# Kernel tuning notes

Hardware: AMD Instinct MI355X
Metric: run time of the kernel (lower is better)

The kernel has to match this reference:

```python
import jax, jax.numpy as jnp
import numpy as np

N_NODES = 100000   # m for both sparse matmuls (graph adjacency is N x N)
ITERATIONS = 10
ALPHA = 0.1
N_FEATURES = 2000
HIDDEN = 64
N_LABELS = 16
NNZ_FEAT = 5000000
N_EDGES = 3200000


def setup_inputs() -> dict:
    key = jax.random.key(0)
    ks = jax.random.split(key, 10)
    feat_rows = jax.random.randint(ks[0], (NNZ_FEAT,), 0, N_NODES, dtype=jnp.int32)
    feat_cols = jax.random.randint(ks[1], (NNZ_FEAT,), 0, N_FEATURES, dtype=jnp.int32)
    feature_values = jax.random.uniform(ks[2], (NNZ_FEAT,), dtype=jnp.float32)
    edge_rows = jax.random.randint(ks[3], (N_EDGES,), 0, N_NODES, dtype=jnp.int32)
    edge_cols = jax.random.randint(ks[4], (N_EDGES,), 0, N_NODES, dtype=jnp.int32)
    edge_weights = jax.random.uniform(ks[5], (N_EDGES,), dtype=jnp.float32) * (1.0 / 32.0)
    W1 = jax.random.normal(ks[6], (N_FEATURES, HIDDEN), dtype=jnp.float32) * 0.05
    b1 = jax.random.normal(ks[7], (HIDDEN,), dtype=jnp.float32) * 0.05
    W2 = jax.random.normal(ks[8], (HIDDEN, N_LABELS), dtype=jnp.float32) * 0.1
    b2 = jax.random.normal(ks[9], (N_LABELS,), dtype=jnp.float32) * 0.1
    return {"feat_rows": feat_rows, "feat_cols": feat_cols, "feature_values": feature_values,
            "edge_rows": edge_rows, "edge_cols": edge_cols, "edge_weights": edge_weights,
            "W1": W1, "b1": b1, "W2": W2, "b2": b2}


def spmm(rows, cols, vals, matrix, m):
    # sparse [m, k] (COO) @ dense [k, d]: gather rows of dense, scale, scatter-add
    out = matrix[cols] * vals[:, None]          # [nnz, d]
    return jax.ops.segment_sum(out, rows, num_segments=m)


def reference(feat_rows, feat_cols, feature_values, edge_rows, edge_cols,
              edge_weights, W1, b1, W2, b2):
    # layer 1: sparse features [N, F] @ W1 [F, H] + b1  (eval mode: dropout is identity)
    latent1 = spmm(feat_rows, feat_cols, feature_values, W1, N_NODES) + b1  # [N, H]
    latent1 = jax.nn.relu(latent1)
    z = latent1 @ W2 + b2                       # [N, L] local predictions

    def step(p, _):
        new = spmm(edge_rows, edge_cols, edge_weights, p, N_NODES)  # A_hat @ p
        p = (1.0 - ALPHA) * new + ALPHA * z
        return p, None

    preds, _ = jax.lax.scan(step, z, None, length=ITERATIONS)
    return jax.nn.log_softmax(preds, axis=1)
```

## Files before the change

### kernel.cpp

```cpp
#include <hip/hip_runtime.h>

#define N_NODES    100000
#define N_FEATURES 2000
#define HIDDEN     64
#define N_LABELS   16
#define NNZ_FEAT   5000000
#define N_EDGES    3200000
#define ITERS      10
#define ALPHA      0.1f

#define CBSH       9
#define CROWS      (1 << CBSH)
#define NBC        ((N_NODES + CROWS - 1) >> CBSH)
#define TILE       8192
#define NFB        ((NNZ_FEAT + TILE - 1) / TILE)
#define NEB        ((N_EDGES + TILE - 1) / TILE)
#define BCAP       28672

#define EQMUL  1048544.0f
#define EWDEC  (0.028125f / 32767.0f)

__device__ __forceinline__ unsigned short f2bf(float x) {
    unsigned u = __float_as_uint(x);
    u += 0x7FFF + ((u >> 16) & 1);
    return (unsigned short)(u >> 16);
}
__device__ __forceinline__ float bf_lo(unsigned u) { return __uint_as_float(u << 16); }
__device__ __forceinline__ float bf_hi(unsigned u) { return __uint_as_float(u & 0xFFFF0000u); }

__device__ __forceinline__ unsigned char f2fp8(float x) {
    float a = fabsf(x) * 16.0f;
    a = fminf(fmaxf(a, 0.015625f), 448.0f);
    unsigned u = __float_as_uint(a) + 0x80000;
    int v11 = (int)((u >> 20) & 0x7FF) - 960;
    v11 = v11 < 8 ? 8 : (v11 > 126 ? 126 : v11);
    return (unsigned char)(v11 | ((__float_as_uint(x) >> 24) & 0x80));
}
#if __has_builtin(__builtin_amdgcn_cvt_f32_fp8)
#define FP8DEC(w, s) __builtin_amdgcn_cvt_f32_fp8((w), (s))
#else
__device__ __forceinline__ float fp8dec_sw(unsigned w, int s) {
    unsigned u = (w >> (8 * s)) & 0xFF;
    return __uint_as_float((((u & 0x7F) + 960) << 20) | ((u & 0x80) << 24));
}
#define FP8DEC(w, s) fp8dec_sw((w), (s))
#endif


__global__ __launch_bounds__(256) void zero_int(int* __restrict__ p, int n) {
    int t = blockIdx.x * 256 + threadIdx.x;
    if (t < n) p[t] = 0;
}

__global__ __launch_bounds__(256) void hist2_k(const int* __restrict__ frows, int nf,
                                               int* __restrict__ cbf,
                                               const int* __restrict__ erows, int ne,
                                               int* __restrict__ cbe) {
    __shared__ int h[NBC];
    for (int i = threadIdx.x; i < NBC; i += 256) h[i] = 0;
    __syncthreads();
    const int* rows; int n; int* dst; int b0, nb;
    if (blockIdx.x < 1280) { rows = frows; n = nf; dst = cbf; b0 = blockIdx.x; nb = 1280; }
    else                   { rows = erows; n = ne; dst = cbe; b0 = blockIdx.x - 1280; nb = 768; }
    int stride = nb * 256;
    for (int i = b0 * 256 + threadIdx.x; i < n; i += stride)
        atomicAdd(&h[rows[i] >> CBSH], 1);
    __syncthreads();
    for (int i = threadIdx.x; i < NBC; i += 256)
        if (h[i]) atomicAdd(&dst[i], h[i]);
}

__global__ __launch_bounds__(256) void scan2_k(const int* __restrict__ cbf,
                                               int* __restrict__ cbasef, int* __restrict__ gbf,
                                               int* __restrict__ frp,
                                               const int* __restrict__ cbe,
                                               int* __restrict__ cbasee, int* __restrict__ gbe,
                                               int* __restrict__ erp) {
    const int* cnt; int* cbase; int* gbcur; int* rp;
    if (blockIdx.x == 0) { cnt = cbf; cbase = cbasef; gbcur = gbf; rp = frp; }
    else                 { cnt = cbe; cbase = cbasee; gbcur = gbe; rp = erp; }
    __shared__ int s[256];
    int t = threadIdx.x;
    int v = (t < NBC) ? cnt[t] : 0;
    s[t] = v;
    __syncthreads();
    for (int off = 1; off < 256; off <<= 1) {
        int a = (t >= off) ? s[t - off] : 0;
        __syncthreads();
        s[t] += a;
        __syncthreads();
    }
    if (t < NBC) { cbase[t] = s[t] - v; gbcur[t] = s[t] - v; }
    if (t == NBC - 1) { cbase[NBC] = s[t]; rp[N_NODES] = s[t]; }
}

__global__ __launch_bounds__(1024) void binA2_k(
    const int* __restrict__ frows, const int* __restrict__ fcols, const float* __restrict__ fvals,
    int* __restrict__ gbf, int* __restrict__ fpk, unsigned short* __restrict__ frl,
    const int* __restrict__ erows, const int* __restrict__ ecols, const float* __restrict__ evals,
    int* __restrict__ gbe, int* __restrict__ epk, unsigned short* __restrict__ erl)
{
    __shared__ int            staged_pk[TILE];
    __shared__ unsigned short staged_rl[TILE];
    __shared__ unsigned char  sbkt[TILE];
    __shared__ int cnt[NBC];
    __shared__ int rstart[NBC];
    __shared__ int gbase[NBC];
    __shared__ int sc[256];

    const int* rows; const int* cols; const float* vals;
    int* gbcur; int* bpk; unsigned short* brl;
    int n, qshift, bfval; float qmul;
    int bid = blockIdx.x;
    if (bid < NFB) {
        rows = frows; cols = fcols; vals = fvals; gbcur = gbf; bpk = fpk; brl = frl;
        n = NNZ_FEAT; qshift = 16; qmul = 0.f; bfval = 1;
    } else {
        bid -= NFB;
        rows = erows; cols = ecols; vals = evals; gbcur = gbe; bpk = epk; brl = erl;
        n = N_EDGES; qshift = 17; qmul = EQMUL; bfval = 0;
    }

    int tid = threadIdx.x;
    int base = bid * TILE;
    int m = n - base; if (m > TILE) m = TILE;

    for (int i = tid; i < NBC; i += 1024) cnt[i] = 0;
    __syncthreads();

    int seq[TILE / 1024];
    int rbuf[TILE / 1024];
    #pragma unroll
    for (int k = 0; k < TILE / 1024; ++k) {
        int j = k * 1024 + tid;
        if (j < m) {
            int r = rows[base + j];
            rbuf[k] = r;
            seq[k] = atomicAdd(&cnt[r >> CBSH], 1);
        }
    }
    __syncthreads();

    if (tid < 256) sc[tid] = (tid < NBC) ? cnt[tid] : 0;
    __syncthreads();
    for (int off = 1; off < 256; off <<= 1) {
        int a = 0;
        if (tid < 256 && tid >= off) a = sc[tid - off];
        __syncthreads();
        if (tid < 256) sc[tid] += a;
        __syncthreads();
    }
    if (tid < NBC) rstart[tid] = sc[tid] - cnt[tid];
    __syncthreads();

    #pragma unroll
    for (int k = 0; k < TILE / 1024; ++k) {
        int j = k * 1024 + tid;
        if (j < m) {
            int r = rbuf[k];
            int b = r >> CBSH;
            float v = vals[base + j];
            int q = bfval ? (int)f2bf(v) : __float2int_rn(v * qmul);
            int slot = rstart[b] + seq[k];
            staged_pk[slot] = (q << qshift) | cols[base + j];
            staged_rl[slot] = (unsigned short)(r & (CROWS - 1));
            sbkt[slot] = (unsigned char)b;
        }
    }
    __syncthreads();

    if (tid < NBC && cnt[tid] > 0) gbase[tid] = atomicAdd(&gbcur[tid], cnt[tid]);
    __syncthreads();

    #pragma unroll
    for (int k = 0; k < TILE / 1024; ++k) {
        int slot = k * 1024 + tid;
        if (slot < m) {
            int b = sbkt[slot];
            int dst = gbase[b] + (slot - rstart[b]);
            bpk[dst] = staged_pk[slot];
            brl[dst] = staged_rl[slot];
        }
    }
}

__global__ __launch_bounds__(1024) void binB3_k(
    const int* __restrict__ fpk, const unsigned short* __restrict__ frl,
    const int* __restrict__ cbasef, int* __restrict__ frp, int* __restrict__ fcw,
    const int* __restrict__ epk, const unsigned short* __restrict__ erl,
    const int* __restrict__ cbasee, int* __restrict__ erp, int* __restrict__ ecw)
{
    const int* bin_pk; const unsigned short* bin_rl; const int* cbase; int* rp; int* cw;
    int b = blockIdx.x;
    if (b < NBC) { bin_pk = fpk; bin_rl = frl; cbase = cbasef; rp = frp; cw = fcw; }
    else { b -= NBC; bin_pk = epk; bin_rl = erl; cbase = cbasee; rp = erp; cw = ecw; }

    int r0 = b << CBSH;
    int nrows = N_NODES - r0; if (nrows > CROWS) nrows = CROWS;
    __shared__ int staged[BCAP];
    __shared__ int hist[CROWS];
    __shared__ int sc[CROWS];
    int t = threadIdx.x;
    if (t < CROWS) hist[t] = 0;
    __syncthreads();
    int s = cbase[b], e = cbase[b + 1];
    int cnt = e - s;
    for (int i = s + t; i < e; i += 1024)
        atomicAdd(&hist[bin_rl[i]], 1);
    __syncthreads();
    if (t < CROWS) sc[t] = hist[t];
    __syncthreads();
    for (int off = 1; off < CROWS; off <<= 1) {
        int a = (t >= off && t < CROWS) ? sc[t - off] : 0;
        __syncthreads();
        if (t < CROWS) sc[t] += a;
        __syncthreads();
    }
    if (t < CROWS) {
        int excl = sc[t] - hist[t];
        if (t < nrows) rp[r0 + t] = excl + s;
        hist[t] = excl;
    }
    __syncthreads();

    if (cnt <= BCAP) {
        for (int i = s + t; i < e; i += 1024) {
            int pos = atomicAdd(&hist[bin_rl[i]], 1);
            staged[pos] = bin_pk[i];
        }
        __syncthreads();
        for (int j = t; j < cnt; j += 1024)
            cw[s + j] = staged[j];
    } else {
        for (int i = s + t; i < e; i += 1024) {
            int pos = atomicAdd(&hist[bin_rl[i]], 1);
            cw[s + pos] = bin_pk[i];
        }
    }
}


__global__ __launch_bounds__(256) void w1_to_fp8(const float* __restrict__ W1,
                                                 unsigned char* __restrict__ W1q) {
    int t = blockIdx.x * 256 + threadIdx.x;
    if (t < N_FEATURES * HIDDEN / 4) {
        float4 v = reinterpret_cast<const float4*>(W1)[t];
        uchar4 o;
        o.x = f2fp8(v.x); o.y = f2fp8(v.y); o.z = f2fp8(v.z); o.w = f2fp8(v.w);
        reinterpret_cast<uchar4*>(W1q)[t] = o;
    }
}

__global__ __launch_bounds__(256) void spmm_fused(const int* __restrict__ rp,
                                                  const int* __restrict__ cwp,
                                                  const unsigned char* __restrict__ W1q,
                                                  const float* __restrict__ b1,
                                                  const float* __restrict__ W2,
                                                  const float* __restrict__ b2,
                                                  unsigned short* __restrict__ az,
                                                  unsigned short* __restrict__ pb0) {
    __shared__ float sW2T[N_LABELS * (HIDDEN + 1)];
    __shared__ float sb1[HIDDEN];
    __shared__ float sb2[N_LABELS];
    for (int i = threadIdx.x; i < HIDDEN * N_LABELS; i += 256) {
        int h = i >> 4, l = i & 15;
        sW2T[l * (HIDDEN + 1) + h] = W2[i];
    }
    if (threadIdx.x < HIDDEN) sb1[threadIdx.x] = b1[threadIdx.x];
    if (threadIdx.x < N_LABELS) sb2[threadIdx.x] = b2[threadIdx.x];
    __syncthreads();

    int t = blockIdx.x * 256 + threadIdx.x;
    int row = t >> 3, sl = t & 7;
    if (row >= N_NODES) return;
    int s = rp[row], e = rp[row + 1];
    int hbase = sl * 8;

    float acc[8];
    #pragma unroll
    for (int j = 0; j < 8; ++j) acc[j] = 0.f;

    int i = s;
    for (; i + 3 < e; i += 4) {
        uint2 wv[4]; float vv[4];
        #pragma unroll
        for (int k = 0; k < 4; ++k) {
            int pk = cwp[i + k];
            vv[k] = bf_hi((unsigned)pk);
            wv[k] = *reinterpret_cast<const uint2*>(W1q + (size_t)(pk & 0x7FF) * HIDDEN + hbase);
        }
        #pragma unroll
        for (int k = 0; k < 4; ++k) {
            acc[0] = fmaf(vv[k], FP8DEC(wv[k].x, 0), acc[0]);
            acc[1] = fmaf(vv[k], FP8DEC(wv[k].x, 1), acc[1]);
            acc[2] = fmaf(vv[k], FP8DEC(wv[k].x, 2), acc[2]);
            acc[3] = fmaf(vv[k], FP8DEC(wv[k].x, 3), acc[3]);
            acc[4] = fmaf(vv[k], FP8DEC(wv[k].y, 0), acc[4]);
            acc[5] = fmaf(vv[k], FP8DEC(wv[k].y, 1), acc[5]);
            acc[6] = fmaf(vv[k], FP8DEC(wv[k].y, 2), acc[6]);
            acc[7] = fmaf(vv[k], FP8DEC(wv[k].y, 3), acc[7]);
        }
    }
    for (; i < e; ++i) {
        int pk = cwp[i];
        float v = bf_hi((unsigned)pk);
        uint2 w = *reinterpret_cast<const uint2*>(W1q + (size_t)(pk & 0x7FF) * HIDDEN + hbase);
        acc[0] = fmaf(v, FP8DEC(w.x, 0), acc[0]);
        acc[1] = fmaf(v, FP8DEC(w.x, 1), acc[1]);
        acc[2] = fmaf(v, FP8DEC(w.x, 2), acc[2]);
        acc[3] = fmaf(v, FP8DEC(w.x, 3), acc[3]);
        acc[4] = fmaf(v, FP8DEC(w.y, 0), acc[4]);
        acc[5] = fmaf(v, FP8DEC(w.y, 1), acc[5]);
        acc[6] = fmaf(v, FP8DEC(w.y, 2), acc[6]);
        acc[7] = fmaf(v, FP8DEC(w.y, 3), acc[7]);
    }

    float part[16];
    #pragma unroll
    for (int l = 0; l < 16; ++l) part[l] = 0.f;
    #pragma unroll
    for (int j = 0; j < 8; ++j) {
        float a = fmaf(acc[j], 0.0625f, sb1[hbase + j]);
        a = a > 0.f ? a : 0.f;
        #pragma unroll
        for (int l = 0; l < 16; ++l)
            part[l] = fmaf(a, sW2T[l * (HIDDEN + 1) + hbase + j], part[l]);
    }
    #pragma unroll
    for (int l = 0; l < 8; ++l) {
        float lo = __shfl_xor(part[l], 1);
        float hi = __shfl_xor(part[l + 8], 1);
        part[l] = (sl & 1) ? (part[l + 8] + hi) : (part[l] + lo);
    }
    #pragma unroll
    for (int l = 0; l < 4; ++l) {
        float lo = __shfl_xor(part[l], 2);
        float hi = __shfl_xor(part[l + 4], 2);
        part[l] = (sl & 2) ? (part[l + 4] + hi) : (part[l] + lo);
    }
    #pragma unroll
    for (int l = 0; l < 2; ++l) {
        float lo = __shfl_xor(part[l], 4);
        float hi = __shfl_xor(part[l + 2], 4);
        part[l] = (sl & 4) ? (part[l + 2] + hi) : (part[l] + lo);
    }
    int lbase = 8 * (sl & 1) + 4 * ((sl >> 1) & 1) + 2 * ((sl >> 2) & 1);
    float z0 = part[0] + sb2[lbase];
    float z1 = part[1] + sb2[lbase + 1];
    unsigned oz = (unsigned)f2bf(z0) | ((unsigned)f2bf(z1) << 16);
    unsigned oa = (unsigned)f2bf(ALPHA * z0) | ((unsigned)f2bf(ALPHA * z1) << 16);
    *reinterpret_cast<unsigned*>(pb0 + (size_t)row * N_LABELS + lbase) = oz;
    *reinterpret_cast<unsigned*>(az  + (size_t)row * N_LABELS + lbase) = oa;
}

__global__ __launch_bounds__(256) void prop_bf16(const int* __restrict__ rp,
                                                 const int* __restrict__ cwp,
                                                 const unsigned short* __restrict__ az,
                                                 const unsigned short* __restrict__ pin,
                                                 unsigned short* __restrict__ pout) {
    int t = blockIdx.x * 256 + threadIdx.x;
    int row = t >> 3, sub = t & 7;
    if (row >= N_NODES) return;
    int s = rp[row], e = rp[row + 1];
    unsigned azw = *reinterpret_cast<const unsigned*>(az + (size_t)row * N_LABELS + sub * 2);
    float a0 = bf_lo(azw), a1 = bf_hi(azw);
    int i = s;
    for (; i + 7 < e; i += 8) {
        int pks[8];
        #pragma unroll
        for (int k = 0; k < 8; ++k) pks[k] = cwp[i + k];
        unsigned q[8]; float w[8];
        #pragma unroll
        for (int k = 0; k < 8; ++k) {
            w[k] = (float)((unsigned)pks[k] >> 17) * EWDEC;
            q[k] = *reinterpret_cast<const unsigned*>(pin + (size_t)(pks[k] & 0x1FFFF) * N_LABELS + sub * 2);
        }
        #pragma unroll
        for (int k = 0; k < 8; ++k) {
            a0 = fmaf(w[k], bf_lo(q[k]), a0);
            a1 = fmaf(w[k], bf_hi(q[k]), a1);
        }
    }
    for (; i < e; ++i) {
        int pk = cwp[i];
        float w = (float)((unsigned)pk >> 17) * EWDEC;
        unsigned q = *reinterpret_cast<const unsigned*>(pin + (size_t)(pk & 0x1FFFF) * N_LABELS + sub * 2);
        a0 = fmaf(w, bf_lo(q), a0);
        a1 = fmaf(w, bf_hi(q), a1);
    }
    *reinterpret_cast<unsigned*>(pout + (size_t)row * N_LABELS + sub * 2) =
        (unsigned)f2bf(a0) | ((unsigned)f2bf(a1) << 16);
}

__global__ __launch_bounds__(256) void prop_final(const int* __restrict__ rp,
                                                  const int* __restrict__ cwp,
                                                  const unsigned short* __restrict__ az,
                                                  const unsigned short* __restrict__ pin,
                                                  float* __restrict__ out) {
    int t = blockIdx.x * 256 + threadIdx.x;
    int row = t >> 3, sub = t & 7;
    if (row >= N_NODES) return;
    int s = rp[row], e = rp[row + 1];
    unsigned azw = *reinterpret_cast<const unsigned*>(az + (size_t)row * N_LABELS + sub * 2);
    float a0 = bf_lo(azw), a1 = bf_hi(azw);
    int i = s;
    for (; i + 7 < e; i += 8) {
        int pks[8];
        #pragma unroll
        for (int k = 0; k < 8; ++k) pks[k] = cwp[i + k];
        unsigned q[8]; float w[8];
        #pragma unroll
        for (int k = 0; k < 8; ++k) {
            w[k] = (float)((unsigned)pks[k] >> 17) * EWDEC;
            q[k] = *reinterpret_cast<const unsigned*>(pin + (size_t)(pks[k] & 0x1FFFF) * N_LABELS + sub * 2);
        }
        #pragma unroll
        for (int k = 0; k < 8; ++k) {
            a0 = fmaf(w[k], bf_lo(q[k]), a0);
            a1 = fmaf(w[k], bf_hi(q[k]), a1);
        }
    }
    for (; i < e; ++i) {
        int pk = cwp[i];
        float w = (float)((unsigned)pk >> 17) * EWDEC;
        unsigned q = *reinterpret_cast<const unsigned*>(pin + (size_t)(pk & 0x1FFFF) * N_LABELS + sub * 2);
        a0 = fmaf(w, bf_lo(q), a0);
        a1 = fmaf(w, bf_hi(q), a1);
    }
    float m = fmaxf(a0, a1);
    m = fmaxf(m, __shfl_xor(m, 1));
    m = fmaxf(m, __shfl_xor(m, 2));
    m = fmaxf(m, __shfl_xor(m, 4));
    float ssum = __expf(a0 - m) + __expf(a1 - m);
    ssum += __shfl_xor(ssum, 1);
    ssum += __shfl_xor(ssum, 2);
    ssum += __shfl_xor(ssum, 4);
    float lse = m + __logf(ssum);
    *reinterpret_cast<float2*>(out + (size_t)row * N_LABELS + sub * 2) =
        make_float2(a0 - lse, a1 - lse);
}


__global__ __launch_bounds__(256) void zero_f4(float4* __restrict__ p, int n4) {
    int t = blockIdx.x * 256 + threadIdx.x;
    if (t < n4) p[t] = make_float4(0.f, 0.f, 0.f, 0.f);
}

__global__ __launch_bounds__(256) void spmm_feat_atomic(
    const int* __restrict__ rows, const int* __restrict__ cols,
    const float* __restrict__ vals, const float* __restrict__ W1,
    float* __restrict__ latent)
{
    long long t = (long long)blockIdx.x * 256 + threadIdx.x;
    if (t >= (long long)NNZ_FEAT * 16) return;
    int e  = (int)(t >> 4);
    int dg = (int)(t & 15);
    int r = rows[e]; int c = cols[e]; float v = vals[e];
    float4 w = *reinterpret_cast<const float4*>(W1 + (size_t)c * HIDDEN + dg * 4);
    float* dst = latent + (size_t)r * HIDDEN + dg * 4;
    atomicAdd(dst + 0, v * w.x); atomicAdd(dst + 1, v * w.y);
    atomicAdd(dst + 2, v * w.z); atomicAdd(dst + 3, v * w.w);
}

__global__ __launch_bounds__(256) void compute_z(const float* __restrict__ latent,
                                                 const float* __restrict__ b1,
                                                 const float* __restrict__ W2,
                                                 const float* __restrict__ b2,
                                                 float* __restrict__ z) {
    __shared__ float sW2[HIDDEN * N_LABELS];
    __shared__ float sb1[HIDDEN];
    for (int i = threadIdx.x; i < HIDDEN * N_LABELS; i += 256) sW2[i] = W2[i];
    if (threadIdx.x < HIDDEN) sb1[threadIdx.x] = b1[threadIdx.x];
    __syncthreads();
    int t = blockIdx.x * 256 + threadIdx.x;
    int node = t >> 4;
    int l = t & 15;
    if (node >= N_NODES) return;
    float acc = b2[l];
    const float* lat = latent + (size_t)node * HIDDEN;
    #pragma unroll 8
    for (int h = 0; h < HIDDEN; ++h) {
        float a = lat[h] + sb1[h];
        a = a > 0.f ? a : 0.f;
        acc = fmaf(a, sW2[h * N_LABELS + l], acc);
    }
    z[(size_t)node * N_LABELS + l] = acc;
}

__global__ __launch_bounds__(256) void init_acc(const float* __restrict__ z,
                                                float* __restrict__ acc) {
    int t = blockIdx.x * 256 + threadIdx.x;
    if (t < N_NODES * N_LABELS / 4) {
        float4 zv = reinterpret_cast<const float4*>(z)[t];
        reinterpret_cast<float4*>(acc)[t] =
            make_float4(ALPHA * zv.x, ALPHA * zv.y, ALPHA * zv.z, ALPHA * zv.w);
    }
}

__global__ __launch_bounds__(256) void edge_scatter(
    const int* __restrict__ rows, const int* __restrict__ cols,
    const float* __restrict__ w, const float* __restrict__ p,
    float* __restrict__ acc)
{
    long long t = (long long)blockIdx.x * 256 + threadIdx.x;
    if (t >= (long long)N_EDGES * 4) return;
    int e = (int)(t >> 2);
    int part = (int)(t & 3);
    int r = rows[e]; int c = cols[e];
    float wt = w[e] * (1.0f - ALPHA);
    float4 pv = *reinterpret_cast<const float4*>(p + (size_t)c * N_LABELS + part * 4);
    float* dst = acc + (size_t)r * N_LABELS + part * 4;
    atomicAdd(dst + 0, wt * pv.x); atomicAdd(dst + 1, wt * pv.y);
    atomicAdd(dst + 2, wt * pv.z); atomicAdd(dst + 3, wt * pv.w);
}

__global__ __launch_bounds__(256) void logsoftmax_k(const float* __restrict__ p,
                                                    float* __restrict__ out) {
    int node = blockIdx.x * 256 + threadIdx.x;
    if (node >= N_NODES) return;
    const float4* src = reinterpret_cast<const float4*>(p + (size_t)node * N_LABELS);
    float4 a = src[0], b = src[1], c = src[2], d = src[3];
    float x[16] = {a.x,a.y,a.z,a.w, b.x,b.y,b.z,b.w, c.x,c.y,c.z,c.w, d.x,d.y,d.z,d.w};
    float m = x[0];
    #pragma unroll
    for (int i = 1; i < 16; ++i) m = fmaxf(m, x[i]);
    float s = 0.f;
    #pragma unroll
    for (int i = 0; i < 16; ++i) s += expf(x[i] - m);
    float lse = m + logf(s);
    float4* o = reinterpret_cast<float4*>(out + (size_t)node * N_LABELS);
    o[0] = make_float4(x[0]-lse,  x[1]-lse,  x[2]-lse,  x[3]-lse);
    o[1] = make_float4(x[4]-lse,  x[5]-lse,  x[6]-lse,  x[7]-lse);
    o[2] = make_float4(x[8]-lse,  x[9]-lse,  x[10]-lse, x[11]-lse);
    o[3] = make_float4(x[12]-lse, x[13]-lse, x[14]-lse, x[15]-lse);
}


extern "C" void kernel_launch(void* const* d_in, const int* in_sizes, int n_in,
                              void* d_out, int out_size, void* d_ws, size_t ws_size,
                              hipStream_t stream)
{
    const int*   feat_rows = (const int*)d_in[0];
    const int*   feat_cols = (const int*)d_in[1];
    const float* feat_vals = (const float*)d_in[2];
    const int*   edge_rows = (const int*)d_in[3];
    const int*   edge_cols = (const int*)d_in[4];
    const float* edge_w    = (const float*)d_in[5];
    const float* W1 = (const float*)d_in[6];
    const float* b1 = (const float*)d_in[7];
    const float* W2 = (const float*)d_in[8];
    const float* b2 = (const float*)d_in[9];
    float* out = (float*)d_out;

    size_t need = 0;
    size_t o_feat_cw = need; need += (size_t)NNZ_FEAT;
    size_t o_edge_cw = need; need += (size_t)N_EDGES;
    size_t o_latent  = need; need += (size_t)N_NODES * HIDDEN;
    size_t o_z       = need; need += (size_t)N_NODES * N_LABELS;
    size_t o_p0      = need; need += (size_t)N_NODES * N_LABELS;
    size_t o_p1      = need; need += (size_t)N_NODES * N_LABELS;
    size_t o_frp     = need; need += N_NODES + 1;
    size_t o_erp     = need; need += N_NODES + 1;
    size_t o_w1q     = need; need += (size_t)N_FEATURES * HIDDEN / 4;
    size_t o_ebin_pk = need; need += (size_t)N_EDGES;
    size_t o_ebin_rl = need; need += (size_t)N_EDGES / 2;
    size_t o_cbf     = need; need += NBC;
    size_t o_cbe     = need; need += NBC;
    size_t o_cbasef  = need; need += NBC + 1;
    size_t o_cbasee  = need; need += NBC + 1;
    size_t o_gbf     = need; need += NBC;
    size_t o_gbe     = need; need += NBC;
    size_t need_bytes = need * 4 + 64;

    float* base = (float*)d_ws;
    float* latent = base + o_latent;
    float* z  = base + o_z;
    float* p0 = base + o_p0;
    float* p1 = base + o_p1;

    if (ws_size >= need_bytes) {
        int* feat_cw = (int*)(base + o_feat_cw);
        int* edge_cw = (int*)(base + o_edge_cw);
        int* feat_rp = (int*)(base + o_frp);
        int* edge_rp = (int*)(base + o_erp);
        unsigned char* W1q = (unsigned char*)(base + o_w1q);
        int* cbf    = (int*)(base + o_cbf);
        int* cbe    = (int*)(base + o_cbe);
        int* cbasef = (int*)(base + o_cbasef);
        int* cbasee = (int*)(base + o_cbasee);
        int* gbf    = (int*)(base + o_gbf);
        int* gbe    = (int*)(base + o_gbe);
        int*            fbin_pk = (int*)(base + o_latent);
        unsigned short* fbin_rl = (unsigned short*)(base + o_z);
        int*            ebin_pk = (int*)(base + o_ebin_pk);
        unsigned short* ebin_rl = (unsigned short*)(base + o_ebin_rl);
        unsigned short* az  = (unsigned short*)z;
        unsigned short* pb0 = (unsigned short*)p0;
        unsigned short* pb1 = (unsigned short*)p1;

        w1_to_fp8<<<(N_FEATURES * HIDDEN / 4 + 255) / 256, 256, 0, stream>>>(W1, W1q);
        zero_int<<<2, 256, 0, stream>>>(cbf, 2 * NBC);
        hist2_k<<<2048, 256, 0, stream>>>(feat_rows, NNZ_FEAT, cbf, edge_rows, N_EDGES, cbe);
        scan2_k<<<2, 256, 0, stream>>>(cbf, cbasef, gbf, feat_rp, cbe, cbasee, gbe, edge_rp);
        binA2_k<<<NFB + NEB, 1024, 0, stream>>>(
            feat_rows, feat_cols, feat_vals, gbf, fbin_pk, fbin_rl,
            edge_rows, edge_cols, edge_w, gbe, ebin_pk, ebin_rl);
        binB3_k<<<2 * NBC, 1024, 0, stream>>>(
            fbin_pk, fbin_rl, cbasef, feat_rp, feat_cw,
            ebin_pk, ebin_rl, cbasee, edge_rp, edge_cw);

        spmm_fused<<<(N_NODES * 8 + 255) / 256, 256, 0, stream>>>(
            feat_rp, feat_cw, W1q, b1, W2, b2, az, pb0);

        const unsigned short* pin = pb0;
        int pgrid = (N_NODES * 8 + 255) / 256;
        for (int it = 0; it < ITERS - 1; ++it) {
            unsigned short* pout = (it & 1) ? pb0 : pb1;
            prop_bf16<<<pgrid, 256, 0, stream>>>(edge_rp, edge_cw, az, pin, pout);
            pin = pout;
        }
        prop_final<<<pgrid, 256, 0, stream>>>(edge_rp, edge_cw, az, pin, out);
    } else {
        int n4 = N_NODES * HIDDEN / 4;
        zero_f4<<<(n4 + 255) / 256, 256, 0, stream>>>((float4*)latent, n4);
        long long total = (long long)NNZ_FEAT * 16;
        spmm_feat_atomic<<<(int)((total + 255) / 256), 256, 0, stream>>>(
            feat_rows, feat_cols, feat_vals, W1, latent);
        compute_z<<<N_NODES * 16 / 256, 256, 0, stream>>>(latent, b1, W2, b2, z);
        const float* pin = z;
        float* bufs[2] = {p0, p1};
        for (int it = 0; it < ITERS; ++it) {
            float* pout = bufs[it & 1];
            init_acc<<<(N_NODES * N_LABELS / 4 + 255) / 256, 256, 0, stream>>>(z, pout);
            long long tot = (long long)N_EDGES * 4;
            edge_scatter<<<(int)((tot + 255) / 256), 256, 0, stream>>>(
                edge_rows, edge_cols, edge_w, pin, pout);
            pin = pout;
        }
        logsoftmax_k<<<(N_NODES + 255) / 256, 256, 0, stream>>>(pin, out);
    }
}
```

Baseline: 459.5 us.

## Split shared atomic counters and share edge loads via intra-group shuffles

The histogram kernel now keeps four replicated shared-memory histograms indexed by thread lane, and the binning kernel splits its per-bucket counters into two copies by thread parity. Both changes spread atomic contention on hot buckets and fold the copies back together when computing offsets. In the propagation kernels, each of the 8 lanes serving a row loads one packed edge word and the words are broadcast with width-8 shuffles, replacing eight redundant per-lane loads. The extra shared memory and shuffle instructions are the cost.

```diff
diff --git a/kernel.cpp b/kernel.cpp
--- a/kernel.cpp
+++ b/kernel.cpp
@@ -56,18 +56,21 @@
                                                int* __restrict__ cbf,
                                                const int* __restrict__ erows, int ne,
                                                int* __restrict__ cbe) {
-    __shared__ int h[NBC];
-    for (int i = threadIdx.x; i < NBC; i += 256) h[i] = 0;
+    __shared__ int h[4 * NBC];
+    for (int i = threadIdx.x; i < 4 * NBC; i += 256) h[i] = 0;
     __syncthreads();
     const int* rows; int n; int* dst; int b0, nb;
     if (blockIdx.x < 1280) { rows = frows; n = nf; dst = cbf; b0 = blockIdx.x; nb = 1280; }
     else                   { rows = erows; n = ne; dst = cbe; b0 = blockIdx.x - 1280; nb = 768; }
+    int off = (threadIdx.x & 3) * NBC;
     int stride = nb * 256;
     for (int i = b0 * 256 + threadIdx.x; i < n; i += stride)
-        atomicAdd(&h[rows[i] >> CBSH], 1);
-    __syncthreads();
-    for (int i = threadIdx.x; i < NBC; i += 256)
-        if (h[i]) atomicAdd(&dst[i], h[i]);
+        atomicAdd(&h[off + (rows[i] >> CBSH)], 1);
+    __syncthreads();
+    for (int i = threadIdx.x; i < NBC; i += 256) {
+        int v = h[i] + h[NBC + i] + h[2 * NBC + i] + h[3 * NBC + i];
+        if (v) atomicAdd(&dst[i], v);
+    }
 }
 
 __global__ __launch_bounds__(256) void scan2_k(const int* __restrict__ cbf,
@@ -103,7 +106,8 @@
     __shared__ int            staged_pk[TILE];
     __shared__ unsigned short staged_rl[TILE];
     __shared__ unsigned char  sbkt[TILE];
-    __shared__ int cnt[NBC];
+    __shared__ int cnt0[NBC];
+    __shared__ int cnt1[NBC];
     __shared__ int rstart[NBC];
     __shared__ int gbase[NBC];
     __shared__ int sc[256];
@@ -125,9 +129,11 @@
     int base = bid * TILE;
     int m = n - base; if (m > TILE) m = TILE;
 
-    for (int i = tid; i < NBC; i += 1024) cnt[i] = 0;
-    __syncthreads();
-
+    for (int i = tid; i < NBC; i += 1024) { cnt0[i] = 0; cnt1[i] = 0; }
+    __syncthreads();
+
+    int c = tid & 1;
+    int* cntc = c ? cnt1 : cnt0;
     int seq[TILE / 1024];
     int rbuf[TILE / 1024];
     #pragma unroll
@@ -136,12 +142,12 @@
         if (j < m) {
             int r = rows[base + j];
             rbuf[k] = r;
-            seq[k] = atomicAdd(&cnt[r >> CBSH], 1);
-        }
-    }
-    __syncthreads();
-
-    if (tid < 256) sc[tid] = (tid < NBC) ? cnt[tid] : 0;
+            seq[k] = atomicAdd(&cntc[r >> CBSH], 1);
+        }
+    }
+    __syncthreads();
+
+    if (tid < 256) sc[tid] = (tid < NBC) ? (cnt0[tid] + cnt1[tid]) : 0;
     __syncthreads();
     for (int off = 1; off < 256; off <<= 1) {
         int a = 0;
@@ -150,7 +156,7 @@
         if (tid < 256) sc[tid] += a;
         __syncthreads();
     }
-    if (tid < NBC) rstart[tid] = sc[tid] - cnt[tid];
+    if (tid < NBC) rstart[tid] = sc[tid] - (cnt0[tid] + cnt1[tid]);
     __syncthreads();
 
     #pragma unroll
@@ -161,7 +167,7 @@
             int b = r >> CBSH;
             float v = vals[base + j];
             int q = bfval ? (int)f2bf(v) : __float2int_rn(v * qmul);
-            int slot = rstart[b] + seq[k];
+            int slot = rstart[b] + (c ? cnt0[b] : 0) + seq[k];
             staged_pk[slot] = (q << qshift) | cols[base + j];
             staged_rl[slot] = (unsigned short)(r & (CROWS - 1));
             sbkt[slot] = (unsigned char)b;
@@ -169,7 +175,10 @@
     }
     __syncthreads();
 
-    if (tid < NBC && cnt[tid] > 0) gbase[tid] = atomicAdd(&gbcur[tid], cnt[tid]);
+    if (tid < NBC) {
+        int tot = cnt0[tid] + cnt1[tid];
+        if (tot > 0) gbase[tid] = atomicAdd(&gbcur[tid], tot);
+    }
     __syncthreads();
 
     #pragma unroll
@@ -366,14 +375,13 @@
     float a0 = bf_lo(azw), a1 = bf_hi(azw);
     int i = s;
     for (; i + 7 < e; i += 8) {
-        int pks[8];
-        #pragma unroll
-        for (int k = 0; k < 8; ++k) pks[k] = cwp[i + k];
+        int cwv = cwp[i + sub];
         unsigned q[8]; float w[8];
         #pragma unroll
         for (int k = 0; k < 8; ++k) {
-            w[k] = (float)((unsigned)pks[k] >> 17) * EWDEC;
-            q[k] = *reinterpret_cast<const unsigned*>(pin + (size_t)(pks[k] & 0x1FFFF) * N_LABELS + sub * 2);
+            int pk = __shfl(cwv, k, 8);
+            w[k] = (float)((unsigned)pk >> 17) * EWDEC;
+            q[k] = *reinterpret_cast<const unsigned*>(pin + (size_t)(pk & 0x1FFFF) * N_LABELS + sub * 2);
         }
         #pragma unroll
         for (int k = 0; k < 8; ++k) {
@@ -405,14 +413,13 @@
     float a0 = bf_lo(azw), a1 = bf_hi(azw);
     int i = s;
     for (; i + 7 < e; i += 8) {
-        int pks[8];
-        #pragma unroll
-        for (int k = 0; k < 8; ++k) pks[k] = cwp[i + k];
+        int cwv = cwp[i + sub];
         unsigned q[8]; float w[8];
         #pragma unroll
         for (int k = 0; k < 8; ++k) {
-            w[k] = (float)((unsigned)pks[k] >> 17) * EWDEC;
-            q[k] = *reinterpret_cast<const unsigned*>(pin + (size_t)(pks[k] & 0x1FFFF) * N_LABELS + sub * 2);
+            int pk = __shfl(cwv, k, 8);
+            w[k] = (float)((unsigned)pk >> 17) * EWDEC;
+            q[k] = *reinterpret_cast<const unsigned*>(pin + (size_t)(pk & 0x1FFFF) * N_LABELS + sub * 2);
         }
         #pragma unroll
         for (int k = 0; k < 8; ++k) {
```

Measured after the change: 461.4 us. No clear change (+0.4%).
